# Optimization experiments

Hardware: AMD Instinct MI355X
Metric: run time of the kernel (lower is better)

The kernel has to match this reference:

```python
import jax, jax.numpy as jnp
import numpy as np

MODEL_DIM = 512
COND_DIM = 768
HEAD_DIM = 64
N_HEADS = 8


def setup_inputs() -> dict:
    key = jax.random.key(0)
    k1, k2, k3, k4, k5, k6 = jax.random.split(key, 6)
    inner = HEAD_DIM * N_HEADS
    x = jax.random.normal(k1, (16, 4096, MODEL_DIM), dtype=jnp.float32)
    cond = jax.random.normal(k2, (16, 77, COND_DIM), dtype=jnp.float32)
    # nn.Linear weights (out, in); apply as x @ W.T
    s = 0.02
    w_q = jax.random.normal(k3, (inner, MODEL_DIM), dtype=jnp.float32) * s
    w_k = jax.random.normal(k4, (inner, COND_DIM), dtype=jnp.float32) * s
    w_v = jax.random.normal(k5, (inner, COND_DIM), dtype=jnp.float32) * s
    w_o = jax.random.normal(k6, (MODEL_DIM, inner), dtype=jnp.float32) * s
    return {"x": x, "cond": cond, "w_q": w_q, "w_k": w_k, "w_v": w_v, "w_o": w_o}


def reference(x, cond, w_q, w_k, w_v, w_o):
    b, lq, _ = x.shape
    lk = cond.shape[1]
    q = (x @ w_q.T).reshape(b, lq, N_HEADS, HEAD_DIM)
    k = (cond @ w_k.T).reshape(b, lk, N_HEADS, HEAD_DIM)
    v = (cond @ w_v.T).reshape(b, lk, N_HEADS, HEAD_DIM)
    scale = HEAD_DIM ** -0.5
    attn = jnp.einsum('bihd,bjhd->bhij', q, k) * scale  # [b,h,lq,lk]
    attn = jax.nn.softmax(attn, axis=-1)
    out = jnp.einsum('bhij,bjhd->bihd', attn, v).reshape(b, lq, N_HEADS * HEAD_DIM)
    return out @ w_o.T
```

## Files before the change

### kernel.cpp

```cpp
#include <hip/hip_runtime.h>
#include <hip/hip_bf16.h>
#include <stdint.h>


typedef __bf16 bf16_t;
typedef __bf16 bf16x8 __attribute__((ext_vector_type(8)));
typedef float floatx4 __attribute__((ext_vector_type(4)));

#define MFMA16(a, b, c) __builtin_amdgcn_mfma_f32_16x16x32_bf16((a), (b), (c), 0, 0, 0)

__device__ __forceinline__ void gload_lds16(const bf16_t* g, bf16_t* l)
{
    __builtin_amdgcn_global_load_lds(
        (const __attribute__((address_space(1))) void*)g,
        (__attribute__((address_space(3))) void*)l, 16, 0, 0);
}

__device__ __forceinline__ void stage_cvt8(const float* g, bf16_t* l)
{
    floatx4 f0 = *(const floatx4*)g;
    floatx4 f1 = *(const floatx4*)(g + 4);
    bf16x8 v;
#pragma unroll
    for (int e = 0; e < 4; e++) { v[e] = (bf16_t)f0[e]; v[e + 4] = (bf16_t)f1[e]; }
    *(bf16x8*)l = v;
}

__device__ __forceinline__ void cvt8(const float* in, bf16_t* out, long long i)
{
    floatx4 f0 = *(const floatx4*)(in + i * 8);
    floatx4 f1 = *(const floatx4*)(in + i * 8 + 4);
    bf16x8 v;
#pragma unroll
    for (int e = 0; e < 4; e++) { v[e] = (bf16_t)f0[e]; v[e + 4] = (bf16_t)f1[e]; }
    *(bf16x8*)(out + i * 8) = v;
}

template <bool AF32, bool CF32>
__global__ __launch_bounds__(256) void gemm_bt(
    const void* __restrict__ Av, const bf16_t* __restrict__ B,
    void* __restrict__ Cv, int M, int N, int K)
{
    __shared__ bf16_t As[2 * 128 * 32];
    __shared__ bf16_t Bs[2 * 128 * 32];

    const int t = threadIdx.x;
    const int l = t & 63;
    const int w = t >> 6;
    const int wm = w >> 1, wn = w & 1;
    const int l15 = l & 15, l4 = l >> 4;

    const int nbx = gridDim.x;
    const int nwg = nbx * gridDim.y;
    int lid = blockIdx.y * nbx + blockIdx.x;
    if ((nwg & 7) == 0) {
        const int cpx = nwg >> 3;
        lid = (lid & 7) * cpx + (lid >> 3);
    }
    const int m0 = (lid / nbx) * 128, n0 = (lid % nbx) * 128;

    floatx4 acc[4][4] = {};

    const float*  agf[4];
    const bf16_t* agb[4];
    const bf16_t* bg[4];
    bf16_t* al[4];
    bf16_t* bl[4];
#pragma unroll
    for (int i = 0; i < 4; i++) {
        int e = (i * 256 + t) * 8;
        int kk = e >> 12;
        int row = (e & 4095) >> 5;
        int col = kk * 32 + (e & 31);
        int ra = m0 + row; if (ra > M - 1) ra = M - 1;
        if (AF32) agf[i] = (const float*)Av + (size_t)ra * K + col;
        else      agb[i] = (const bf16_t*)Av + (size_t)ra * K + col;
        bg[i] = B + (size_t)(n0 + row) * K + col;
        al[i] = &As[e];
        bl[i] = &Bs[e];
    }

    for (int k0 = 0; k0 < K; k0 += 64) {
#pragma unroll
        for (int i = 0; i < 4; i++) {
            if (AF32) stage_cvt8(agf[i] + k0, al[i]);
            else      gload_lds16(agb[i] + k0, al[i]);
            gload_lds16(bg[i] + k0, bl[i]);
        }
        __syncthreads();

#pragma unroll
        for (int kk = 0; kk < 2; kk++) {
            bf16x8 af[4], bfr[4];
#pragma unroll
            for (int i = 0; i < 4; i++)
                af[i] = *(const bf16x8*)&As[kk * 4096 + (wm * 64 + i * 16 + l15) * 32 + l4 * 8];
#pragma unroll
            for (int j = 0; j < 4; j++)
                bfr[j] = *(const bf16x8*)&Bs[kk * 4096 + (wn * 64 + j * 16 + l15) * 32 + l4 * 8];
#pragma unroll
            for (int i = 0; i < 4; i++)
#pragma unroll
                for (int j = 0; j < 4; j++)
                    acc[i][j] = MFMA16(af[i], bfr[j], acc[i][j]);
        }
        __syncthreads();
    }

#pragma unroll
    for (int i = 0; i < 4; i++)
#pragma unroll
        for (int j = 0; j < 4; j++)
#pragma unroll
            for (int r = 0; r < 4; r++) {
                int row = m0 + wm * 64 + i * 16 + l4 * 4 + r;
                int col = n0 + wn * 64 + j * 16 + l15;
                if (row < M) {
                    if (CF32) ((float*)Cv)[(size_t)row * N + col] = acc[i][j][r];
                    else ((bf16_t*)Cv)[(size_t)row * N + col] = (bf16_t)acc[i][j][r];
                }
            }
}

__global__ __launch_bounds__(256) void prep(
    const float* __restrict__ cond, const float* __restrict__ w_k,
    const float* __restrict__ w_v, const float* __restrict__ w_q,
    const float* __restrict__ w_o, bf16_t* __restrict__ KVb,
    bf16_t* __restrict__ Wqb, bf16_t* __restrict__ Wob)
{
    __shared__ bf16_t As[2 * 128 * 32];
    __shared__ bf16_t Bs[2 * 128 * 32];

    const int bid = blockIdx.x;
    const int t = threadIdx.x;

    if (bid >= 80) {
        if (bid < 208) cvt8(w_q, Wqb, (long long)(bid - 80) * 256 + t);
        else           cvt8(w_o, Wob, (long long)(bid - 208) * 256 + t);
        return;
    }

    const int l = t & 63;
    const int w = t >> 6;
    const int wm = w >> 1, wn = w & 1;
    const int l15 = l & 15, l4 = l >> 4;
    const int m0 = (bid >> 3) * 128, n0 = (bid & 7) * 128;
    const int M = 1232, K = 768;

    floatx4 acc[4][4] = {};

    const float* ag[4];
    const float* bg[4];
    bf16_t* al[4];
    bf16_t* bl[4];
#pragma unroll
    for (int i = 0; i < 4; i++) {
        int e = (i * 256 + t) * 8;
        int kk = e >> 12;
        int row = (e & 4095) >> 5;
        int col = kk * 32 + (e & 31);
        int ra = m0 + row; if (ra > M - 1) ra = M - 1;
        ag[i] = cond + (size_t)ra * K + col;
        int rb = n0 + row;
        bg[i] = (rb < 512 ? w_k + (size_t)rb * K
                          : w_v + (size_t)(rb - 512) * K) + col;
        al[i] = &As[e];
        bl[i] = &Bs[e];
    }

    for (int k0 = 0; k0 < K; k0 += 64) {
#pragma unroll
        for (int i = 0; i < 4; i++) {
            stage_cvt8(ag[i] + k0, al[i]);
            stage_cvt8(bg[i] + k0, bl[i]);
        }
        __syncthreads();

#pragma unroll
        for (int kk = 0; kk < 2; kk++) {
            bf16x8 af[4], bfr[4];
#pragma unroll
            for (int i = 0; i < 4; i++)
                af[i] = *(const bf16x8*)&As[kk * 4096 + (wm * 64 + i * 16 + l15) * 32 + l4 * 8];
#pragma unroll
            for (int j = 0; j < 4; j++)
                bfr[j] = *(const bf16x8*)&Bs[kk * 4096 + (wn * 64 + j * 16 + l15) * 32 + l4 * 8];
#pragma unroll
            for (int i = 0; i < 4; i++)
#pragma unroll
                for (int j = 0; j < 4; j++)
                    acc[i][j] = MFMA16(af[i], bfr[j], acc[i][j]);
        }
        __syncthreads();
    }

#pragma unroll
    for (int i = 0; i < 4; i++)
#pragma unroll
        for (int j = 0; j < 4; j++)
#pragma unroll
            for (int r = 0; r < 4; r++) {
                int row = m0 + wm * 64 + i * 16 + l4 * 4 + r;
                int col = n0 + wn * 64 + j * 16 + l15;
                if (row < M)
                    KVb[(size_t)row * 1024 + col] = (bf16_t)acc[i][j][r];
            }
}

#define LK 77
#define KVSTR 1024
#define KSTR 72
#define VSTR 104
#define JP 96

__global__ __launch_bounds__(256) void attn_fused(
    bf16_t* QO,
    const bf16_t* __restrict__ KVg)
{
    __shared__ bf16_t Ks[80 * KSTR];
    __shared__ bf16_t Vs[64 * VSTR];
    __shared__ bf16_t Ps[4 * 32 * VSTR];

    const int t = threadIdx.x;
    const int w = t >> 6, l = t & 63;
    const int l15 = l & 15, l4 = l >> 4;
    const int b = blockIdx.y >> 3, h = blockIdx.y & 7;
    const int q0 = blockIdx.x * 128;

    const bf16_t* qbase =
        QO + ((size_t)(b * 4096 + q0 + w * 32 + l15)) * 512 + h * 64 + l4 * 8;
    bf16x8 aq[2][2];
    aq[0][0] = *(const bf16x8*)qbase;
    aq[0][1] = *(const bf16x8*)(qbase + 32);
    aq[1][0] = *(const bf16x8*)(qbase + 16 * 512);
    aq[1][1] = *(const bf16x8*)(qbase + 16 * 512 + 32);

    const bf16_t* Kg = KVg;
    const bf16_t* Vg = KVg + 512;

    for (int idx = t; idx < LK * 8; idx += 256) {
        int j = idx >> 3, c = (idx & 7) * 8;
        *(uint4*)&Ks[j * KSTR + c] =
            *(const uint4*)&Kg[((size_t)(b * LK + j)) * KVSTR + h * 64 + c];
    }
    for (int idx = t; idx < 3 * KSTR; idx += 256)
        Ks[LK * KSTR + idx] = (bf16_t)0.0f;

    for (int u = t; u < LK * 8; u += 256) {
        int j = u >> 3, d0 = (u & 7) * 8;
        uint4 pk = *(const uint4*)&Vg[((size_t)(b * LK + j)) * KVSTR + h * 64 + d0];
        const bf16_t* pv = (const bf16_t*)&pk;
#pragma unroll
        for (int e = 0; e < 8; e++)
            Vs[(d0 + e) * VSTR + j] = pv[e];
    }
    for (int idx = t; idx < 64 * (JP - LK); idx += 256) {
        int d = idx / (JP - LK), j = LK + idx % (JP - LK);
        Vs[d * VSTR + j] = (bf16_t)0.0f;
    }
    __syncthreads();

    floatx4 s[2][5];
    __builtin_amdgcn_s_setprio(1);
#pragma unroll
    for (int n = 0; n < 5; n++) {
        bf16x8 b0 = *(const bf16x8*)&Ks[(n * 16 + l15) * KSTR + l4 * 8];
        bf16x8 b1 = *(const bf16x8*)&Ks[(n * 16 + l15) * KSTR + 32 + l4 * 8];
#pragma unroll
        for (int mi = 0; mi < 2; mi++) {
            floatx4 z = {0.f, 0.f, 0.f, 0.f};
            z = MFMA16(aq[mi][0], b0, z);
            z = MFMA16(aq[mi][1], b1, z);
            s[mi][n] = z;
        }
    }
    __builtin_amdgcn_s_setprio(0);

    const float scale = 0.125f;
    float p[2][5][4], linv[2][4];
#pragma unroll
    for (int mi = 0; mi < 2; mi++)
#pragma unroll
        for (int r = 0; r < 4; r++) {
            float smax = -1e30f;
#pragma unroll
            for (int n = 0; n < 5; n++) {
                float v = s[mi][n][r] * scale;
                if (n == 4 && (64 + l15) >= LK) v = -1e30f;
                p[mi][n][r] = v;
                smax = fmaxf(smax, v);
            }
#pragma unroll
            for (int off = 1; off < 16; off <<= 1)
                smax = fmaxf(smax, __shfl_xor(smax, off, 64));
            float sum = 0.f;
#pragma unroll
            for (int n = 0; n < 5; n++) {
                float e2 = __expf(p[mi][n][r] - smax);
                p[mi][n][r] = e2;
                sum += e2;
            }
#pragma unroll
            for (int off = 1; off < 16; off <<= 1)
                sum += __shfl_xor(sum, off, 64);
            linv[mi][r] = 1.0f / sum;
        }

    bf16_t* pw = Ps + w * 32 * VSTR;
#pragma unroll
    for (int mi = 0; mi < 2; mi++)
#pragma unroll
        for (int r = 0; r < 4; r++) {
            int row = mi * 16 + l4 * 4 + r;
#pragma unroll
            for (int n = 0; n < 5; n++)
                pw[row * VSTR + n * 16 + l15] = (bf16_t)(p[mi][n][r] * linv[mi][r]);
            pw[row * VSTR + 80 + l15] = (bf16_t)0.0f;
        }
    __syncthreads();

    bf16x8 ap[2][3];
#pragma unroll
    for (int mi = 0; mi < 2; mi++)
#pragma unroll
        for (int ks = 0; ks < 3; ks++)
            ap[mi][ks] = *(const bf16x8*)&pw[(mi * 16 + l15) * VSTR + ks * 32 + l4 * 8];
#pragma unroll
    for (int n2 = 0; n2 < 4; n2++) {
        bf16x8 bv[3];
#pragma unroll
        for (int ks = 0; ks < 3; ks++)
            bv[ks] = *(const bf16x8*)&Vs[(n2 * 16 + l15) * VSTR + ks * 32 + l4 * 8];
        floatx4 o[2];
        __builtin_amdgcn_s_setprio(1);
#pragma unroll
        for (int mi = 0; mi < 2; mi++) {
            floatx4 z = {0.f, 0.f, 0.f, 0.f};
#pragma unroll
            for (int ks = 0; ks < 3; ks++)
                z = MFMA16(ap[mi][ks], bv[ks], z);
            o[mi] = z;
        }
        __builtin_amdgcn_s_setprio(0);
#pragma unroll
        for (int mi = 0; mi < 2; mi++)
#pragma unroll
            for (int r = 0; r < 4; r++) {
                int q = q0 + w * 32 + mi * 16 + l4 * 4 + r;
                QO[((size_t)(b * 4096 + q)) * 512 + h * 64 + n2 * 16 + l15] =
                    (bf16_t)o[mi][r];
            }
    }
}

extern "C" void kernel_launch(void* const* d_in, const int* in_sizes, int n_in,
                              void* d_out, int out_size, void* d_ws, size_t ws_size,
                              hipStream_t stream)
{
    const float* x    = (const float*)d_in[0];
    const float* cond = (const float*)d_in[1];
    const float* w_q  = (const float*)d_in[2];
    const float* w_k  = (const float*)d_in[3];
    const float* w_v  = (const float*)d_in[4];
    const float* w_o  = (const float*)d_in[5];
    float* out = (float*)d_out;

    const int Mq  = 16 * 4096;
    const int Mkv = 16 * 77;

    bf16_t* Qb  = (bf16_t*)d_ws;
    bf16_t* KVb = Qb  + (size_t)Mq * 512;
    bf16_t* Wqb = KVb + (size_t)Mkv * 1024;
    bf16_t* Wob = Wqb + (size_t)512 * 512;

    prep<<<dim3(336), 256, 0, stream>>>(cond, w_k, w_v, w_q, w_o, KVb, Wqb, Wob);

    gemm_bt<true, false><<<dim3(4, Mq / 128), 256, 0, stream>>>(x, Wqb, Qb, Mq, 512, 512);

    attn_fused<<<dim3(32, 128), 256, 0, stream>>>(Qb, KVb);

    gemm_bt<false, true><<<dim3(4, Mq / 128), 256, 0, stream>>>(Qb, Wob, out, Mq, 512, 512);
}
```

Before: 398.6 us.

## Double-buffer LDS tiles in gemm_bt to overlap global loads with MFMA

Converts the GEMM main loop from a single LDS buffer with two barriers per k-step into a ping-pong double buffer. The next tile is prefetched while MFMAs run on the current one; for fp32 A the loads go to registers and are converted and stored after compute. This aims to hide global load latency and drop one barrier per iteration, at the cost of twice the LDS (64KB per block), which may reduce occupancy. It also raises wave priority around the MFMA block and hardcodes K=768 in the prep kernel loop.

```diff
diff --git a/kernel.cpp b/kernel.cpp
--- a/kernel.cpp
+++ b/kernel.cpp
@@ -35,14 +35,16 @@
     for (int e = 0; e < 4; e++) { v[e] = (bf16_t)f0[e]; v[e + 4] = (bf16_t)f1[e]; }
     *(bf16x8*)(out + i * 8) = v;
 }
+
+#define TSZ (2 * 128 * 32)
 
 template <bool AF32, bool CF32>
 __global__ __launch_bounds__(256) void gemm_bt(
     const void* __restrict__ Av, const bf16_t* __restrict__ B,
     void* __restrict__ Cv, int M, int N, int K)
 {
-    __shared__ bf16_t As[2 * 128 * 32];
-    __shared__ bf16_t Bs[2 * 128 * 32];
+    __shared__ bf16_t As[2 * TSZ];
+    __shared__ bf16_t Bs[2 * TSZ];
 
     const int t = threadIdx.x;
     const int l = t & 63;
@@ -64,8 +66,7 @@
     const float*  agf[4];
     const bf16_t* agb[4];
     const bf16_t* bg[4];
-    bf16_t* al[4];
-    bf16_t* bl[4];
+    int eo[4];
 #pragma unroll
     for (int i = 0; i < 4; i++) {
         int e = (i * 256 + t) * 8;
@@ -76,35 +77,78 @@
         if (AF32) agf[i] = (const float*)Av + (size_t)ra * K + col;
         else      agb[i] = (const bf16_t*)Av + (size_t)ra * K + col;
         bg[i] = B + (size_t)(n0 + row) * K + col;
-        al[i] = &As[e];
-        bl[i] = &Bs[e];
-    }
-
-    for (int k0 = 0; k0 < K; k0 += 64) {
-#pragma unroll
-        for (int i = 0; i < 4; i++) {
-            if (AF32) stage_cvt8(agf[i] + k0, al[i]);
-            else      gload_lds16(agb[i] + k0, al[i]);
-            gload_lds16(bg[i] + k0, bl[i]);
-        }
+        eo[i] = e;
+    }
+
+#pragma unroll
+    for (int i = 0; i < 4; i++) {
+        if (AF32) stage_cvt8(agf[i], &As[eo[i]]);
+        else      gload_lds16(agb[i], &As[eo[i]]);
+        gload_lds16(bg[i], &Bs[eo[i]]);
+    }
+    __syncthreads();
+
+    const int nt = K >> 6;
+    int cur = 0;
+    for (int tt = 0; tt < nt; ++tt) {
+        const int kn = (tt + 1) << 6;
+        const int nxt = (cur ^ 1) * TSZ;
+        const bool more = (tt + 1 < nt);
+
+        floatx4 pf0[4], pf1[4];
+        if (more) {
+            if (AF32) {
+#pragma unroll
+                for (int i = 0; i < 4; i++) {
+                    pf0[i] = *(const floatx4*)(agf[i] + kn);
+                    pf1[i] = *(const floatx4*)(agf[i] + kn + 4);
+                }
+            } else {
+#pragma unroll
+                for (int i = 0; i < 4; i++)
+                    gload_lds16(agb[i] + kn, &As[nxt + eo[i]]);
+            }
+#pragma unroll
+            for (int i = 0; i < 4; i++)
+                gload_lds16(bg[i] + kn, &Bs[nxt + eo[i]]);
+        }
+
+        const int cb = cur * TSZ;
+        bf16x8 af[2][4], bfr[2][4];
+#pragma unroll
+        for (int kk = 0; kk < 2; kk++) {
+#pragma unroll
+            for (int i = 0; i < 4; i++) {
+                af[kk][i]  = *(const bf16x8*)&As[cb + kk * 4096 + (wm * 64 + i * 16 + l15) * 32 + l4 * 8];
+                bfr[kk][i] = *(const bf16x8*)&Bs[cb + kk * 4096 + (wn * 64 + i * 16 + l15) * 32 + l4 * 8];
+            }
+        }
+
+        __builtin_amdgcn_s_setprio(1);
+#pragma unroll
+        for (int kk = 0; kk < 2; kk++)
+#pragma unroll
+            for (int i = 0; i < 4; i++)
+#pragma unroll
+                for (int j = 0; j < 4; j++)
+                    acc[i][j] = MFMA16(af[kk][i], bfr[kk][j], acc[i][j]);
+        __builtin_amdgcn_s_setprio(0);
+
+        if (AF32 && more) {
+#pragma unroll
+            for (int i = 0; i < 4; i++) {
+                bf16x8 v;
+#pragma unroll
+                for (int e = 0; e < 4; e++) {
+                    v[e]     = (bf16_t)pf0[i][e];
+                    v[e + 4] = (bf16_t)pf1[i][e];
+                }
+                *(bf16x8*)&As[nxt + eo[i]] = v;
+            }
+        }
+
         __syncthreads();
-
-#pragma unroll
-        for (int kk = 0; kk < 2; kk++) {
-            bf16x8 af[4], bfr[4];
-#pragma unroll
-            for (int i = 0; i < 4; i++)
-                af[i] = *(const bf16x8*)&As[kk * 4096 + (wm * 64 + i * 16 + l15) * 32 + l4 * 8];
-#pragma unroll
-            for (int j = 0; j < 4; j++)
-                bfr[j] = *(const bf16x8*)&Bs[kk * 4096 + (wn * 64 + j * 16 + l15) * 32 + l4 * 8];
-#pragma unroll
-            for (int i = 0; i < 4; i++)
-#pragma unroll
-                for (int j = 0; j < 4; j++)
-                    acc[i][j] = MFMA16(af[i], bfr[j], acc[i][j]);
-        }
-        __syncthreads();
+        cur ^= 1;
     }
 
 #pragma unroll
@@ -168,7 +212,7 @@
         bl[i] = &Bs[e];
     }
 
-    for (int k0 = 0; k0 < K; k0 += 64) {
+    for (int k0 = 0; k0 < 768; k0 += 64) {
 #pragma unroll
         for (int i = 0; i < 4; i++) {
             stage_cvt8(ag[i] + k0, al[i]);
```

Measured after the change: 398.9 us. No clear change (+0.1%).
